# Kernel optimization log

Measured on AMD Instinct MI355X. Metric: run time of the kernel, lower is better.

The kernel has to match this reference:

```python
import jax, jax.numpy as jnp
import numpy as np

MUL = 64      # multiplicity of each irrep (64x0e + 64x1o)
B = 8192      # batch / number of nodes
INV_SQRT3 = float(1.0 / np.sqrt(3.0))  # e3nn wigner_3j normalization for (1,1,0),(0,1,1),(1,0,1)
# component normalization: alpha = sqrt(dim_out / fan_in), fan_in = sum over paths of mul_u*mul_v
FAN_IN = 2 * MUL * MUL  # two paths feed each output irrep
ALPHA0 = float(np.sqrt(1.0 / FAN_IN))  # l_out = 0, dim 1
ALPHA1 = float(np.sqrt(3.0 / FAN_IN))  # l_out = 1, dim 3


def setup_inputs() -> dict:
    key = jax.random.key(0)
    kx, k0, k1, k2, k3 = jax.random.split(key, 5)
    x = jax.random.normal(kx, (B, 4 * MUL), dtype=jnp.float32)  # [B, 64*1 + 64*3]
    w000 = jax.random.normal(k0, (MUL, MUL, MUL), dtype=jnp.float32)  # 0e x 0e -> 0e
    w110 = jax.random.normal(k1, (MUL, MUL, MUL), dtype=jnp.float32)  # 1o x 1o -> 0e
    w011 = jax.random.normal(k2, (MUL, MUL, MUL), dtype=jnp.float32)  # 0e x 1o -> 1o
    w101 = jax.random.normal(k3, (MUL, MUL, MUL), dtype=jnp.float32)  # 1o x 0e -> 1o
    return {"x": x, "w000": w000, "w110": w110, "w011": w011, "w101": w101}


def reference(x, w000, w110, w011, w101):
    # split concatenated irrep features: scalars then vectors
    x0 = x[:, :MUL]                          # [B, U]      l=0 (e)
    x1 = x[:, MUL:].reshape(-1, MUL, 3)      # [B, U, 3]   l=1 (o)

    # path (0e,0e)->0e : CG = 1
    p000 = jnp.einsum('uvw,bu,bv->bw', w000, x0, x0)
    # path (1o,1o)->0e : CG[i,j] = delta_ij / sqrt(3)
    p110 = jnp.einsum('uvw,bui,bvi->bw', w110, x1, x1) * INV_SQRT3
    out0 = ALPHA0 * (p000 + p110)            # [B, W]

    # path (0e,1o)->1o : CG[j,k] = delta_jk / sqrt(3)
    p011 = jnp.einsum('uvw,bu,bvk->bwk', w011, x0, x1) * INV_SQRT3
    # path (1o,0e)->1o : CG[i,k] = delta_ik / sqrt(3)
    p101 = jnp.einsum('uvw,buk,bv->bwk', w101, x1, x0) * INV_SQRT3
    out1 = ALPHA1 * (p011 + p101)            # [B, W, 3]

    return jnp.concatenate([out0, out1.reshape(out1.shape[0], MUL * 3)], axis=-1)
```

## Files before the change

### kernel.cpp

```cpp
#include <hip/hip_runtime.h>
#include <hip/hip_bf16.h>
#include <cstdint>

#define BM 32
#define NTHREADS 320
#define WS_TILE 524288
#define WBUF_BYTES 24576
#define SMEM_BYTES (2*WBUF_BYTES + 4*64*32*4)

typedef __bf16 bf16x8_t __attribute__((ext_vector_type(8)));
typedef float f32x4_t __attribute__((ext_vector_type(4)));

__device__ __forceinline__ void async_ld16(const void* g, void* l) {
  __builtin_amdgcn_global_load_lds((const __attribute__((address_space(1))) unsigned int*)g,
                                   (__attribute__((address_space(3))) unsigned int*)l,
                                   16, 0, 0);
}

__global__ __launch_bounds__(256) void prep_weights(const float* __restrict__ w000,
                                                    const float* __restrict__ w110,
                                                    const float* __restrict__ w011,
                                                    const float* __restrict__ w101,
                                                    char* __restrict__ ws) {
  const float A0  = 0.011048543456039806f;
  const float A0I = A0 * 0.57735026918962576f;
  int t = blockIdx.x * 256 + threadIdx.x;
  int u = t >> 9, c = (t >> 6) & 7, w = t & 63;
  bf16x8_t p0, p1, pc;
#pragma unroll
  for (int j = 0; j < 8; ++j) {
    int v = 8 * c + j;
    float a = w000[u * 4096 + v * 64 + w] * A0;
    float b = w110[u * 4096 + v * 64 + w] * A0I;
    float d = (w011[u * 4096 + v * 64 + w] + w101[v * 4096 + u * 64 + w]) * A0;
    p0[j] = (__bf16)a;
    p1[j] = (__bf16)b;
    pc[j] = (__bf16)d;
  }
  int off = ((w * 128 + 16 * c) ^ ((w & 7) << 4)) + u * 8192;
  *(bf16x8_t*)(ws + off) = p0;
  *(bf16x8_t*)(ws + WS_TILE + off) = p1;
  *(bf16x8_t*)(ws + 2 * WS_TILE + off) = pc;
}

__global__ __launch_bounds__(NTHREADS) void tp_main(const float* __restrict__ x,
                                                    const char* __restrict__ ws,
                                                    float* __restrict__ out) {
  extern __shared__ char smem[];
  float* xS = (float*)(smem + 2 * WBUF_BYTES);
  const int tid = threadIdx.x;
  const int wave = tid >> 6, lane = tid & 63;
  const int lr = lane & 15, lg = lane >> 4;
  const int b0 = blockIdx.x * BM;
  const int role = wave;

  if (wave < 3) {
    const char* g = ws + wave * WS_TILE + lane * 16;
#pragma unroll
    for (int c = 0; c < 8; ++c)
      async_ld16(g + c * 1024, smem + wave * 8192 + c * 1024);
  }

  for (int idx = tid; idx < 4 * 64 * 32; idx += NTHREADS) {
    int vec = idx >> 11, rem = idx & 2047;
    int uu = rem >> 5, bb = rem & 31;
    int col = (vec == 0) ? uu : (64 + 3 * uu + (vec - 1));
    xS[idx] = x[(b0 + bb) * 256 + col];
  }

  float xp[3][2][2][8];
  if (role == 1) {
#pragma unroll
    for (int vi = 0; vi < 3; ++vi)
#pragma unroll
      for (int m = 0; m < 2; ++m)
#pragma unroll
        for (int kf = 0; kf < 2; ++kf)
#pragma unroll
          for (int j = 0; j < 8; ++j) {
            int v = 8 * lg + 32 * kf + j;
            xp[vi][m][kf][j] = x[(b0 + 16 * m + lr) * 256 + 64 + 3 * v + vi];
          }
  } else {
    const int vsel = (role == 0) ? 0 : (role - 1);
#pragma unroll
    for (int m = 0; m < 2; ++m)
#pragma unroll
      for (int kf = 0; kf < 2; ++kf)
#pragma unroll
        for (int j = 0; j < 8; ++j) {
          int v = 8 * lg + 32 * kf + j;
          int col = (vsel == 0) ? v : (64 + 3 * v + (vsel - 1));
          xp[0][m][kf][j] = x[(b0 + 16 * m + lr) * 256 + col];
        }
  }

  f32x4_t acc[2][4];
#pragma unroll
  for (int m = 0; m < 2; ++m)
#pragma unroll
    for (int n = 0; n < 4; ++n) {
      f32x4_t z = {0.f, 0.f, 0.f, 0.f};
      acc[m][n] = z;
    }

  __syncthreads();

  const int tsel = (role == 0) ? 0 : ((role == 1) ? 1 : 2);
  int cur = 0;
  for (int u = 0; u < 64; ++u) {
    if (u < 63 && wave < 3) {
      const char* g = ws + wave * WS_TILE + (u + 1) * 8192 + lane * 16;
#pragma unroll
      for (int c = 0; c < 8; ++c)
        async_ld16(g + c * 1024, smem + (cur ^ 1) * WBUF_BYTES + wave * 8192 + c * 1024);
    }

    const char* wt = smem + cur * WBUF_BYTES + tsel * 8192;
    bf16x8_t bfr[4][2];
#pragma unroll
    for (int n = 0; n < 4; ++n)
#pragma unroll
      for (int kf = 0; kf < 2; ++kf) {
        int wrow = 16 * n + lr;
        int off = ((wrow * 128 + (8 * lg + 32 * kf) * 2) ^ ((wrow & 7) << 4));
        bfr[n][kf] = *(const bf16x8_t*)(wt + off);
      }

    bf16x8_t afr[2][2];
    if (role == 1) {
      float s0a = xS[1 * 2048 + u * 32 + lr],      s1a = xS[2 * 2048 + u * 32 + lr],      s2a = xS[3 * 2048 + u * 32 + lr];
      float s0b = xS[1 * 2048 + u * 32 + 16 + lr], s1b = xS[2 * 2048 + u * 32 + 16 + lr], s2b = xS[3 * 2048 + u * 32 + 16 + lr];
#pragma unroll
      for (int kf = 0; kf < 2; ++kf)
#pragma unroll
        for (int j = 0; j < 8; ++j) {
          afr[0][kf][j] = (__bf16)(s0a * xp[0][0][kf][j] + s1a * xp[1][0][kf][j] + s2a * xp[2][0][kf][j]);
          afr[1][kf][j] = (__bf16)(s0b * xp[0][1][kf][j] + s1b * xp[1][1][kf][j] + s2b * xp[2][1][kf][j]);
        }
    } else {
      float sa = xS[u * 32 + lr], sb = xS[u * 32 + 16 + lr];
#pragma unroll
      for (int kf = 0; kf < 2; ++kf)
#pragma unroll
        for (int j = 0; j < 8; ++j) {
          afr[0][kf][j] = (__bf16)(sa * xp[0][0][kf][j]);
          afr[1][kf][j] = (__bf16)(sb * xp[0][1][kf][j]);
        }
    }

#pragma unroll
    for (int m = 0; m < 2; ++m)
#pragma unroll
      for (int n = 0; n < 4; ++n)
#pragma unroll
        for (int kf = 0; kf < 2; ++kf)
          acc[m][n] = __builtin_amdgcn_mfma_f32_16x16x32_bf16(afr[m][kf], bfr[n][kf], acc[m][n], 0, 0, 0);

    __syncthreads();
    cur ^= 1;
  }

  float* pscr = (float*)smem;
  if (role == 1) {
#pragma unroll
    for (int m = 0; m < 2; ++m)
#pragma unroll
      for (int n = 0; n < 4; ++n)
#pragma unroll
        for (int r = 0; r < 4; ++r)
          pscr[(16 * m + 4 * lg + r) * 64 + 16 * n + lr] = acc[m][n][r];
  }
  __syncthreads();
  if (role == 0) {
#pragma unroll
    for (int m = 0; m < 2; ++m)
#pragma unroll
      for (int n = 0; n < 4; ++n)
#pragma unroll
        for (int r = 0; r < 4; ++r) {
          int row = 16 * m + 4 * lg + r, col = 16 * n + lr;
          out[(b0 + row) * 256 + col] = acc[m][n][r] + pscr[row * 64 + col];
        }
  } else if (role >= 2) {
    const int k = role - 2;
#pragma unroll
    for (int m = 0; m < 2; ++m)
#pragma unroll
      for (int n = 0; n < 4; ++n)
#pragma unroll
        for (int r = 0; r < 4; ++r) {
          int row = 16 * m + 4 * lg + r, col = 16 * n + lr;
          out[(b0 + row) * 256 + 64 + 3 * col + k] = acc[m][n][r];
        }
  }
}

extern "C" void kernel_launch(void* const* d_in, const int* in_sizes, int n_in,
                              void* d_out, int out_size, void* d_ws, size_t ws_size,
                              hipStream_t stream) {
  const float* x    = (const float*)d_in[0];
  const float* w000 = (const float*)d_in[1];
  const float* w110 = (const float*)d_in[2];
  const float* w011 = (const float*)d_in[3];
  const float* w101 = (const float*)d_in[4];
  float* out = (float*)d_out;
  char* ws = (char*)d_ws;

  prep_weights<<<128, 256, 0, stream>>>(w000, w110, w011, w101, ws);

  hipFuncSetAttribute((const void*)tp_main, hipFuncAttributeMaxDynamicSharedMemorySize, SMEM_BYTES);
  tp_main<<<256, NTHREADS, SMEM_BYTES, stream>>>(x, ws, out);
}
```

Baseline: 59.64 us.

## Load weight fragments directly from global into registers with triple-buffered prefetch

Drops the LDS double-buffered async staging of the per-u weight tiles and the per-iteration __syncthreads. The prep kernel now writes weights in MFMA fragment order so each lane reads its B fragments with coalesced 16-byte global loads straight into registers. A three-deep register ring overlaps those loads with the MFMA work of earlier steps. This adds register pressure (launch bounds of 1 block per CU) and relies on L2 hits for weights re-read by every block.

```diff
diff --git a/kernel.cpp b/kernel.cpp
--- a/kernel.cpp
+++ b/kernel.cpp
@@ -5,17 +5,9 @@
 #define BM 32
 #define NTHREADS 320
 #define WS_TILE 524288
-#define WBUF_BYTES 24576
-#define SMEM_BYTES (2*WBUF_BYTES + 4*64*32*4)
 
 typedef __bf16 bf16x8_t __attribute__((ext_vector_type(8)));
 typedef float f32x4_t __attribute__((ext_vector_type(4)));
-
-__device__ __forceinline__ void async_ld16(const void* g, void* l) {
-  __builtin_amdgcn_global_load_lds((const __attribute__((address_space(1))) unsigned int*)g,
-                                   (__attribute__((address_space(3))) unsigned int*)l,
-                                   16, 0, 0);
-}
 
 __global__ __launch_bounds__(256) void prep_weights(const float* __restrict__ w000,
                                                     const float* __restrict__ w110,
@@ -25,11 +17,14 @@
   const float A0  = 0.011048543456039806f;
   const float A0I = A0 * 0.57735026918962576f;
   int t = blockIdx.x * 256 + threadIdx.x;
-  int u = t >> 9, c = (t >> 6) & 7, w = t & 63;
+  int u = t >> 9, f = (t >> 6) & 7, l = t & 63;
+  int n = f >> 1, kf = f & 1;
+  int w = 16 * n + (l & 15);
+  int vbase = 8 * (l >> 4) + 32 * kf;
   bf16x8_t p0, p1, pc;
 #pragma unroll
   for (int j = 0; j < 8; ++j) {
-    int v = 8 * c + j;
+    int v = vbase + j;
     float a = w000[u * 4096 + v * 64 + w] * A0;
     float b = w110[u * 4096 + v * 64 + w] * A0I;
     float d = (w011[u * 4096 + v * 64 + w] + w101[v * 4096 + u * 64 + w]) * A0;
@@ -37,29 +32,23 @@
     p1[j] = (__bf16)b;
     pc[j] = (__bf16)d;
   }
-  int off = ((w * 128 + 16 * c) ^ ((w & 7) << 4)) + u * 8192;
+  int off = u * 8192 + f * 1024 + l * 16;
   *(bf16x8_t*)(ws + off) = p0;
   *(bf16x8_t*)(ws + WS_TILE + off) = p1;
   *(bf16x8_t*)(ws + 2 * WS_TILE + off) = pc;
 }
 
-__global__ __launch_bounds__(NTHREADS) void tp_main(const float* __restrict__ x,
-                                                    const char* __restrict__ ws,
-                                                    float* __restrict__ out) {
-  extern __shared__ char smem[];
-  float* xS = (float*)(smem + 2 * WBUF_BYTES);
+__global__ __launch_bounds__(NTHREADS, 1) void tp_main(const float* __restrict__ x,
+                                                       const char* __restrict__ ws,
+                                                       float* __restrict__ out) {
+  __shared__ float xS[4 * 64 * 32];
   const int tid = threadIdx.x;
   const int wave = tid >> 6, lane = tid & 63;
   const int lr = lane & 15, lg = lane >> 4;
   const int b0 = blockIdx.x * BM;
   const int role = wave;
-
-  if (wave < 3) {
-    const char* g = ws + wave * WS_TILE + lane * 16;
-#pragma unroll
-    for (int c = 0; c < 8; ++c)
-      async_ld16(g + c * 1024, smem + wave * 8192 + c * 1024);
-  }
+  const int tsel = (role == 0) ? 0 : ((role == 1) ? 1 : 2);
+  const bf16x8_t* wb = (const bf16x8_t*)(ws + tsel * WS_TILE) + lane;
 
   for (int idx = tid; idx < 4 * 64 * 32; idx += NTHREADS) {
     int vec = idx >> 11, rem = idx & 2047;
@@ -106,31 +95,16 @@
 
   __syncthreads();
 
-  const int tsel = (role == 0) ? 0 : ((role == 1) ? 1 : 2);
-  int cur = 0;
-  for (int u = 0; u < 64; ++u) {
-    if (u < 63 && wave < 3) {
-      const char* g = ws + wave * WS_TILE + (u + 1) * 8192 + lane * 16;
-#pragma unroll
-      for (int c = 0; c < 8; ++c)
-        async_ld16(g + c * 1024, smem + (cur ^ 1) * WBUF_BYTES + wave * 8192 + c * 1024);
-    }
-
-    const char* wt = smem + cur * WBUF_BYTES + tsel * 8192;
-    bf16x8_t bfr[4][2];
-#pragma unroll
-    for (int n = 0; n < 4; ++n)
-#pragma unroll
-      for (int kf = 0; kf < 2; ++kf) {
-        int wrow = 16 * n + lr;
-        int off = ((wrow * 128 + (8 * lg + 32 * kf) * 2) ^ ((wrow & 7) << 4));
-        bfr[n][kf] = *(const bf16x8_t*)(wt + off);
-      }
-
+  auto LOADF = [&](bf16x8_t (&Bb)[8], int uu) {
+#pragma unroll
+    for (int f = 0; f < 8; ++f) Bb[f] = wb[uu * 512 + f * 64];
+  };
+
+  auto STEP = [&](bf16x8_t (&Bb)[8], int uu) {
     bf16x8_t afr[2][2];
     if (role == 1) {
-      float s0a = xS[1 * 2048 + u * 32 + lr],      s1a = xS[2 * 2048 + u * 32 + lr],      s2a = xS[3 * 2048 + u * 32 + lr];
-      float s0b = xS[1 * 2048 + u * 32 + 16 + lr], s1b = xS[2 * 2048 + u * 32 + 16 + lr], s2b = xS[3 * 2048 + u * 32 + 16 + lr];
+      float s0a = xS[1 * 2048 + uu * 32 + lr],      s1a = xS[2 * 2048 + uu * 32 + lr],      s2a = xS[3 * 2048 + uu * 32 + lr];
+      float s0b = xS[1 * 2048 + uu * 32 + 16 + lr], s1b = xS[2 * 2048 + uu * 32 + 16 + lr], s2b = xS[3 * 2048 + uu * 32 + 16 + lr];
 #pragma unroll
       for (int kf = 0; kf < 2; ++kf)
 #pragma unroll
@@ -139,7 +113,7 @@
           afr[1][kf][j] = (__bf16)(s0b * xp[0][1][kf][j] + s1b * xp[1][1][kf][j] + s2b * xp[2][1][kf][j]);
         }
     } else {
-      float sa = xS[u * 32 + lr], sb = xS[u * 32 + 16 + lr];
+      float sa = xS[uu * 32 + lr], sb = xS[uu * 32 + 16 + lr];
 #pragma unroll
       for (int kf = 0; kf < 2; ++kf)
 #pragma unroll
@@ -148,20 +122,35 @@
           afr[1][kf][j] = (__bf16)(sb * xp[0][1][kf][j]);
         }
     }
-
 #pragma unroll
     for (int m = 0; m < 2; ++m)
 #pragma unroll
       for (int n = 0; n < 4; ++n)
 #pragma unroll
         for (int kf = 0; kf < 2; ++kf)
-          acc[m][n] = __builtin_amdgcn_mfma_f32_16x16x32_bf16(afr[m][kf], bfr[n][kf], acc[m][n], 0, 0, 0);
-
-    __syncthreads();
-    cur ^= 1;
-  }
-
-  float* pscr = (float*)smem;
+          acc[m][n] = __builtin_amdgcn_mfma_f32_16x16x32_bf16(afr[m][kf], Bb[n * 2 + kf], acc[m][n], 0, 0, 0);
+  };
+
+  bf16x8_t B0[8], B1[8], B2[8];
+  LOADF(B0, 0);
+  LOADF(B1, 1);
+  for (int u = 0; u < 60; u += 3) {
+    LOADF(B2, u + 2);
+    STEP(B0, u);
+    LOADF(B0, u + 3);
+    STEP(B1, u + 1);
+    LOADF(B1, u + 4);
+    STEP(B2, u + 2);
+  }
+  LOADF(B2, 62);
+  STEP(B0, 60);
+  LOADF(B0, 63);
+  STEP(B1, 61);
+  STEP(B2, 62);
+  STEP(B0, 63);
+
+  __syncthreads();
+  float* pscr = xS;
   if (role == 1) {
 #pragma unroll
     for (int m = 0; m < 2; ++m)
@@ -208,7 +197,5 @@
   char* ws = (char*)d_ws;
 
   prep_weights<<<128, 256, 0, stream>>>(w000, w110, w011, w101, ws);
-
-  hipFuncSetAttribute((const void*)tp_main, hipFuncAttributeMaxDynamicSharedMemorySize, SMEM_BYTES);
-  tp_main<<<256, NTHREADS, SMEM_BYTES, stream>>>(x, ws, out);
+  tp_main<<<256, NTHREADS, 0, stream>>>(x, ws, out);
 }
```

Measured after the change: 102.9 us. +72.5%, slower.
